# Performance work log

Hardware: AMD Instinct MI355X
Metric: run time of the kernel (lower is better)

Reference implementation:

```python
import jax, jax.numpy as jnp
import numpy as np

SLIDING_WINDOW = 512
LOGIT_SOFTCAP = 50.0
NEG_INF = -1e30


def setup_inputs() -> dict:
    key = jax.random.key(0)
    ks = jax.random.split(key, 3)
    B, S, H, KVH, D, BS = 4, 1024, 32, 8, 128, 64
    nb = S // BS          # blocks per sequence = 16
    nblocks = B * nb      # total cache blocks = 64
    total = B * S         # flattened tokens = 4096
    return {
        "query": jax.random.normal(ks[0], (total, H, D), dtype=jnp.float32),
        "key": jax.random.normal(ks[1], (total, KVH, D), dtype=jnp.float32),
        "value": jax.random.normal(ks[2], (total, KVH, D), dtype=jnp.float32),
        "k_cache": jnp.zeros((nblocks, BS, KVH, D), dtype=jnp.float32),
        "v_cache": jnp.zeros((nblocks, BS, KVH, D), dtype=jnp.float32),
        "block_offsets": jnp.arange(nblocks, dtype=jnp.int32).reshape(B, nb),
    }


def reference(query, key, value, k_cache, v_cache, block_offsets):
    B, nb = block_offsets.shape
    nblocks, BS, KVH, D = k_cache.shape
    S = nb * BS
    H = query.shape[1]
    G = H // KVH  # GQA group size
    scale = D ** -0.5

    flat_blocks = block_offsets.reshape(-1)  # [B*nb]
    # 1) write new keys/values into the paged cache per the block table
    k_cache = k_cache.at[flat_blocks].set(key.reshape(-1, BS, KVH, D))
    v_cache = v_cache.at[flat_blocks].set(value.reshape(-1, BS, KVH, D))
    # 2) gather per-sequence contiguous K/V from cache blocks
    k = k_cache[flat_blocks].reshape(B, S, KVH, D)
    v = v_cache[flat_blocks].reshape(B, S, KVH, D)

    q = query.reshape(B, S, KVH, G, D)
    scores = jnp.einsum("bqhgd,bkhd->bhgqk", q, k) * scale
    # logit softcapping (Gemma-style)
    scores = jnp.tanh(scores / LOGIT_SOFTCAP) * LOGIT_SOFTCAP
    # causal + sliding-window mask
    i = jnp.arange(S)[:, None]
    j = jnp.arange(S)[None, :]
    mask = (j <= i) & ((i - j) < SLIDING_WINDOW)
    scores = jnp.where(mask, scores, NEG_INF)
    p = jax.nn.softmax(scores, axis=-1)
    out = jnp.einsum("bhgqk,bkhd->bqhgd", p, v)
    return out.reshape(B * S, H, D)
```

## Files before the change

kernel.cpp:

```cpp
#include <hip/hip_runtime.h>
#include <hip/hip_bf16.h>

typedef __bf16 bf16_t;
typedef bf16_t bf16x8 __attribute__((ext_vector_type(8)));
typedef bf16_t bf16x4 __attribute__((ext_vector_type(4)));
typedef float f32x4 __attribute__((ext_vector_type(4)));

#define B_   4
#define S_   1024
#define H_   32
#define KVH_ 8
#define D_   128
#define WIN_ 512
#define KVD_ (KVH_ * D_)
#define LOG2E_ 1.4426950408889634f
#define C1_ (2.0f * (0.08838834764831845f / 50.0f) * LOG2E_)
#define K2_ (50.0f * LOG2E_)
#define NK22_ (-2.0f * K2_)
#define EXP2F_(x) __builtin_amdgcn_exp2f(x)

__global__ __launch_bounds__(256) void prep_kv(
    const float* __restrict__ K, const float* __restrict__ V,
    bf16_t* __restrict__ Kb, bf16_t* __restrict__ Vt)
{
  const int j0  = blockIdx.x * 64;
  const int kvh = blockIdx.y;
  const int b   = blockIdx.z;
  const int t   = threadIdx.x;
  const int j   = t >> 2;
  const int d0  = (t & 3) * 32;
  __shared__ bf16_t tl[128][72];

  {
    const float* src = K + (size_t)(b * S_ + j0 + j) * KVD_ + kvh * D_ + d0;
    bf16_t* dst = Kb + ((size_t)(b * KVH_ + kvh) * S_ + j0 + j) * D_ + d0;
    #pragma unroll
    for (int c = 0; c < 4; ++c) {
      float4 f0 = *(const float4*)(src + c * 8);
      float4 f1 = *(const float4*)(src + c * 8 + 4);
      bf16x8 o = { (bf16_t)f0.x, (bf16_t)f0.y, (bf16_t)f0.z, (bf16_t)f0.w,
                   (bf16_t)f1.x, (bf16_t)f1.y, (bf16_t)f1.z, (bf16_t)f1.w };
      *(bf16x8*)(dst + c * 8) = o;
    }
  }
  {
    const float* src = V + (size_t)(b * S_ + j0 + j) * KVD_ + kvh * D_ + d0;
    #pragma unroll
    for (int c = 0; c < 8; ++c) {
      float4 f = *(const float4*)(src + c * 4);
      tl[d0 + c * 4 + 0][j] = (bf16_t)f.x;
      tl[d0 + c * 4 + 1][j] = (bf16_t)f.y;
      tl[d0 + c * 4 + 2][j] = (bf16_t)f.z;
      tl[d0 + c * 4 + 3][j] = (bf16_t)f.w;
    }
  }
  __syncthreads();
  {
    const int d = t >> 1, half = (t & 1) * 32;
    bf16_t* dst = Vt + ((size_t)(b * KVH_ + kvh) * D_ + d) * S_ + j0 + half;
    #pragma unroll
    for (int c = 0; c < 4; ++c)
      *(bf16x8*)(dst + c * 8) = *(bf16x8*)&tl[d][half + c * 8];
  }
}

__global__ __launch_bounds__(512, 4) void attn_fwd(
    const float* __restrict__ Q, const bf16_t* __restrict__ Kb,
    const bf16_t* __restrict__ Vt, float* __restrict__ Out)
{
  const int fid = blockIdx.x + 32 * (blockIdx.y + 8 * (int)blockIdx.z);
  const int swz = (fid & 7) * 128 + (fid >> 3);
  const int i0  = (swz & 31) * 32;
  const int kvh = (swz >> 5) & 7;
  const int b   = swz >> 8;

  const int tid  = threadIdx.x;
  const int w    = tid >> 6;
  const int lane = tid & 63;
  const int m16  = lane & 15;
  const int quad = lane >> 4;
  const int g    = w & 3;
  const int rb   = w >> 2;
  const int h    = kvh * 4 + g;
  const int iw   = i0 + rb * 16;
  const int i    = iw + m16;
  const int sw16 = (m16 >> 1) & 3;

  __shared__ __align__(16) bf16_t KsB[2][32 * 128];
  __shared__ __align__(16) bf16_t VtB[2][128 * 32];
  __shared__ __align__(16) bf16_t PsB[8 * 16 * 32];

  bf16x8 qf[4];
  {
    const float* qp = Q + ((size_t)(b * S_ + iw + m16) * H_ + h) * D_;
    #pragma unroll
    for (int s = 0; s < 4; ++s) {
      const int d0 = 32 * s + 8 * quad;
      float4 f0 = *(const float4*)(qp + d0);
      float4 f1 = *(const float4*)(qp + d0 + 4);
      bf16x8 t = { (bf16_t)f0.x, (bf16_t)f0.y, (bf16_t)f0.z, (bf16_t)f0.w,
                   (bf16_t)f1.x, (bf16_t)f1.y, (bf16_t)f1.z, (bf16_t)f1.w };
      qf[s] = t;
    }
  }

  f32x4 O[8];
  #pragma unroll
  for (int c = 0; c < 8; ++c) O[c] = (f32x4){0.f, 0.f, 0.f, 0.f};
  f32x4 lacc = (f32x4){0.f, 0.f, 0.f, 0.f};

  const bf16_t* khead = Kb + (size_t)(b * KVH_ + kvh) * S_ * D_;
  const bf16_t* vhead = Vt + (size_t)(b * KVH_ + kvh) * D_ * S_;

  const int krow = tid >> 4, kpos = tid & 15;
  const int vd   = tid >> 2, vpos = tid & 3;
  const bf16_t* ksrc = khead + (size_t)krow * D_ + kpos * 8;
  const bf16_t* vsrc = vhead + (size_t)vd * S_ + vpos * 8;
  const int koff = krow * 128 + ((kpos ^ (krow & 15)) << 3);
  const int voff = vd * 32 + ((vpos ^ ((vd >> 1) & 3)) << 3);

  const int t_lo = (i0 >= WIN_) ? ((i0 - (WIN_ - 1)) >> 5) : 0;
  const int t_hi = i0 >> 5;

  {
    int4 kr = *(const int4*)(ksrc + (size_t)t_lo * 32 * D_);
    int4 vr = *(const int4*)(vsrc + t_lo * 32);
    *(int4*)&KsB[0][koff] = kr;
    *(int4*)&VtB[0][voff] = vr;
  }
  __syncthreads();
  int buf = 0;

  for (int tb = t_lo; tb <= t_hi; ++tb) {
    const int j0  = tb * 32;
    const bool pre = (tb < t_hi);
    int4 kr, vr;
    if (pre) {
      kr = *(const int4*)(ksrc + (size_t)(j0 + 32) * D_);
      vr = *(const int4*)(vsrc + (j0 + 32));
    }

    if (!(j0 > iw + 15 || j0 + 31 < iw - (WIN_ - 1))) {
      const bool full = (j0 + 31 <= iw) && (iw + 15 - j0 < WIN_);
      const int pw = w * (16 * 32);

      #pragma unroll
      for (int t4 = 0; t4 < 2; ++t4) {
        f32x4 acc = (f32x4){0.f, 0.f, 0.f, 0.f};
        const int row = 16 * t4 + m16;
        __builtin_amdgcn_s_setprio(1);
        #pragma unroll
        for (int s = 0; s < 4; ++s) {
          bf16x8 a = *(const bf16x8*)&KsB[buf][row * 128 + (((quad + 4 * s) ^ m16) << 3)];
          acc = __builtin_amdgcn_mfma_f32_16x16x32_bf16(a, qf[s], acc, 0, 0, 0);
        }
        __builtin_amdgcn_s_setprio(0);
        bf16x4 pk;
        #pragma unroll
        for (int r = 0; r < 4; ++r) {
          float ez = EXP2F_(acc[r] * C1_);
          float p  = EXP2F_(NK22_ * __builtin_amdgcn_rcpf(ez + 1.f));
          if (!full) {
            const int j = j0 + t4 * 16 + 4 * quad + r;
            p = ((j <= i) && (i - j < WIN_)) ? p : 0.f;
          }
          lacc[r] += p;
          pk[r] = (bf16_t)p;
        }
        const int ch = (2 * t4 + (quad >> 1)) ^ sw16;
        *(bf16x4*)&PsB[pw + m16 * 32 + ch * 8 + (quad & 1) * 4] = pk;
      }
      bf16x8 pa = *(const bf16x8*)&PsB[pw + m16 * 32 + ((quad ^ sw16) << 3)];

      __builtin_amdgcn_s_setprio(1);
      #pragma unroll
      for (int c = 0; c < 8; ++c) {
        const int vrow = 16 * c + m16;
        bf16x8 v = *(const bf16x8*)&VtB[buf][vrow * 32 + ((quad ^ sw16) << 3)];
        O[c] = __builtin_amdgcn_mfma_f32_16x16x32_bf16(pa, v, O[c], 0, 0, 0);
      }
      __builtin_amdgcn_s_setprio(0);
    }

    if (pre) {
      *(int4*)&KsB[buf ^ 1][koff] = kr;
      *(int4*)&VtB[buf ^ 1][voff] = vr;
    }
    __syncthreads();
    buf ^= 1;
  }

  float l_run = lacc[0] + lacc[1] + lacc[2] + lacc[3];
  l_run += __shfl_xor(l_run, 16);
  l_run += __shfl_xor(l_run, 32);

  float* ob = Out + ((size_t)(b * S_ + iw) * H_ + h) * D_;
  #pragma unroll
  for (int r = 0; r < 4; ++r) {
    const int rr = 4 * quad + r;
    const float lr = __shfl(l_run, rr);
    const float linv = __builtin_amdgcn_rcpf(lr);
    float* po = ob + (size_t)rr * (H_ * D_);
    #pragma unroll
    for (int c = 0; c < 8; ++c) po[c * 16 + m16] = O[c][r] * linv;
  }
}

extern "C" void kernel_launch(void* const* d_in, const int* in_sizes, int n_in,
                              void* d_out, int out_size, void* d_ws, size_t ws_size,
                              hipStream_t stream) {
  const float* q = (const float*)d_in[0];
  const float* k = (const float*)d_in[1];
  const float* v = (const float*)d_in[2];
  float* out = (float*)d_out;
  const size_t nkv = (size_t)B_ * KVH_ * S_ * D_;
  bf16_t *kb, *vt;
  if (ws_size >= 2 * nkv * sizeof(bf16_t)) {
    kb = (bf16_t*)d_ws; vt = kb + nkv;
  } else {
    kb = (bf16_t*)d_in[3]; vt = (bf16_t*)d_in[4];
  }
  prep_kv<<<dim3(S_ / 64, KVH_, B_), 256, 0, stream>>>(k, v, kb, vt);
  attn_fwd<<<dim3(S_ / 32, KVH_, B_), 512, 0, stream>>>(q, kb, vt, out);
}
```

Measured before the change: 210.7 us.

## Fuse K/V bf16 conversion and V transpose into attention kernel loads

Removes the separate prep_kv kernel and has the attention kernel read fp32 K and V directly from global memory. Half the threads convert K tiles and half convert and transpose V tiles into swizzled shared memory, and the PV read swizzle is adjusted to match. This saves a kernel launch and the bf16 workspace round trip. In exchange, each attention block now re-reads and re-converts fp32 K/V (twice the bytes of bf16) across the window, and the V stores become narrow 2-element LDS writes.

```diff
diff --git a/kernel.cpp b/kernel.cpp
--- a/kernel.cpp
+++ b/kernel.cpp
@@ -4,6 +4,7 @@
 typedef __bf16 bf16_t;
 typedef bf16_t bf16x8 __attribute__((ext_vector_type(8)));
 typedef bf16_t bf16x4 __attribute__((ext_vector_type(4)));
+typedef bf16_t bf16x2 __attribute__((ext_vector_type(2)));
 typedef float f32x4 __attribute__((ext_vector_type(4)));
 
 #define B_   4
@@ -19,54 +20,9 @@
 #define NK22_ (-2.0f * K2_)
 #define EXP2F_(x) __builtin_amdgcn_exp2f(x)
 
-__global__ __launch_bounds__(256) void prep_kv(
-    const float* __restrict__ K, const float* __restrict__ V,
-    bf16_t* __restrict__ Kb, bf16_t* __restrict__ Vt)
-{
-  const int j0  = blockIdx.x * 64;
-  const int kvh = blockIdx.y;
-  const int b   = blockIdx.z;
-  const int t   = threadIdx.x;
-  const int j   = t >> 2;
-  const int d0  = (t & 3) * 32;
-  __shared__ bf16_t tl[128][72];
-
-  {
-    const float* src = K + (size_t)(b * S_ + j0 + j) * KVD_ + kvh * D_ + d0;
-    bf16_t* dst = Kb + ((size_t)(b * KVH_ + kvh) * S_ + j0 + j) * D_ + d0;
-    #pragma unroll
-    for (int c = 0; c < 4; ++c) {
-      float4 f0 = *(const float4*)(src + c * 8);
-      float4 f1 = *(const float4*)(src + c * 8 + 4);
-      bf16x8 o = { (bf16_t)f0.x, (bf16_t)f0.y, (bf16_t)f0.z, (bf16_t)f0.w,
-                   (bf16_t)f1.x, (bf16_t)f1.y, (bf16_t)f1.z, (bf16_t)f1.w };
-      *(bf16x8*)(dst + c * 8) = o;
-    }
-  }
-  {
-    const float* src = V + (size_t)(b * S_ + j0 + j) * KVD_ + kvh * D_ + d0;
-    #pragma unroll
-    for (int c = 0; c < 8; ++c) {
-      float4 f = *(const float4*)(src + c * 4);
-      tl[d0 + c * 4 + 0][j] = (bf16_t)f.x;
-      tl[d0 + c * 4 + 1][j] = (bf16_t)f.y;
-      tl[d0 + c * 4 + 2][j] = (bf16_t)f.z;
-      tl[d0 + c * 4 + 3][j] = (bf16_t)f.w;
-    }
-  }
-  __syncthreads();
-  {
-    const int d = t >> 1, half = (t & 1) * 32;
-    bf16_t* dst = Vt + ((size_t)(b * KVH_ + kvh) * D_ + d) * S_ + j0 + half;
-    #pragma unroll
-    for (int c = 0; c < 4; ++c)
-      *(bf16x8*)(dst + c * 8) = *(bf16x8*)&tl[d][half + c * 8];
-  }
-}
-
 __global__ __launch_bounds__(512, 4) void attn_fwd(
-    const float* __restrict__ Q, const bf16_t* __restrict__ Kb,
-    const bf16_t* __restrict__ Vt, float* __restrict__ Out)
+    const float* __restrict__ Q, const float* __restrict__ K,
+    const float* __restrict__ V, float* __restrict__ Out)
 {
   const int fid = blockIdx.x + 32 * (blockIdx.y + 8 * (int)blockIdx.z);
   const int swz = (fid & 7) * 128 + (fid >> 3);
@@ -109,36 +65,62 @@
   for (int c = 0; c < 8; ++c) O[c] = (f32x4){0.f, 0.f, 0.f, 0.f};
   f32x4 lacc = (f32x4){0.f, 0.f, 0.f, 0.f};
 
-  const bf16_t* khead = Kb + (size_t)(b * KVH_ + kvh) * S_ * D_;
-  const bf16_t* vhead = Vt + (size_t)(b * KVH_ + kvh) * D_ * S_;
-
-  const int krow = tid >> 4, kpos = tid & 15;
-  const int vd   = tid >> 2, vpos = tid & 3;
-  const bf16_t* ksrc = khead + (size_t)krow * D_ + kpos * 8;
-  const bf16_t* vsrc = vhead + (size_t)vd * S_ + vpos * 8;
-  const int koff = krow * 128 + ((kpos ^ (krow & 15)) << 3);
-  const int voff = vd * 32 + ((vpos ^ ((vd >> 1) & 3)) << 3);
+  const bool isK = (tid < 256);
+  const int krow = tid >> 3;
+  const int kseg = tid & 7;
+  const float* ksrc = K + ((size_t)(b * S_ + krow) * KVH_ + kvh) * D_ + kseg * 16;
+  const int koff0 = krow * 128 + (((2 * kseg)     ^ (krow & 15)) << 3);
+  const int koff1 = krow * 128 + (((2 * kseg + 1) ^ (krow & 15)) << 3);
+  const int vt  = tid & 255;
+  const int tv  = (vt >> 4) * 2;
+  const int mpr = vt & 15;
+  const float* vsrc = V + ((size_t)(b * S_ + tv) * KVH_ + kvh) * D_ + mpr * 8;
+  const int vbase = mpr * 256 + (tv & 7);
+  const int vch   = (tv >> 3) ^ ((mpr >> 1) & 3);
 
   const int t_lo = (i0 >= WIN_) ? ((i0 - (WIN_ - 1)) >> 5) : 0;
   const int t_hi = i0 >> 5;
 
-  {
-    int4 kr = *(const int4*)(ksrc + (size_t)t_lo * 32 * D_);
-    int4 vr = *(const int4*)(vsrc + t_lo * 32);
-    *(int4*)&KsB[0][koff] = kr;
-    *(int4*)&VtB[0][voff] = vr;
-  }
+  float4 r0, r1, r2, r3;
+  auto loadStage = [&](int j0v) {
+    if (isK) {
+      const float* p = ksrc + (size_t)j0v * KVD_;
+      r0 = *(const float4*)(p);      r1 = *(const float4*)(p + 4);
+      r2 = *(const float4*)(p + 8);  r3 = *(const float4*)(p + 12);
+    } else {
+      const float* p = vsrc + (size_t)j0v * KVD_;
+      r0 = *(const float4*)(p);            r1 = *(const float4*)(p + 4);
+      r2 = *(const float4*)(p + KVD_);     r3 = *(const float4*)(p + KVD_ + 4);
+    }
+  };
+  auto writeStage = [&](int bi) {
+    if (isK) {
+      bf16x8 lo = { (bf16_t)r0.x, (bf16_t)r0.y, (bf16_t)r0.z, (bf16_t)r0.w,
+                    (bf16_t)r1.x, (bf16_t)r1.y, (bf16_t)r1.z, (bf16_t)r1.w };
+      bf16x8 hi = { (bf16_t)r2.x, (bf16_t)r2.y, (bf16_t)r2.z, (bf16_t)r2.w,
+                    (bf16_t)r3.x, (bf16_t)r3.y, (bf16_t)r3.z, (bf16_t)r3.w };
+      *(bf16x8*)&KsB[bi][koff0] = lo;
+      *(bf16x8*)&KsB[bi][koff1] = hi;
+    } else {
+      const float av[8] = { r0.x, r0.y, r0.z, r0.w, r1.x, r1.y, r1.z, r1.w };
+      const float bv[8] = { r2.x, r2.y, r2.z, r2.w, r3.x, r3.y, r3.z, r3.w };
+      #pragma unroll
+      for (int e = 0; e < 8; ++e) {
+        bf16x2 pr = { (bf16_t)av[e], (bf16_t)bv[e] };
+        *(bf16x2*)&VtB[bi][vbase + e * 32 + ((vch ^ (e >> 1)) << 3)] = pr;
+      }
+    }
+  };
+
+  loadStage(t_lo * 32);
+  writeStage(0);
   __syncthreads();
   int buf = 0;
 
   for (int tb = t_lo; tb <= t_hi; ++tb) {
     const int j0  = tb * 32;
     const bool pre = (tb < t_hi);
-    int4 kr, vr;
-    if (pre) {
-      kr = *(const int4*)(ksrc + (size_t)(j0 + 32) * D_);
-      vr = *(const int4*)(vsrc + (j0 + 32));
-    }
+    if (pre) loadStage(j0 + 32);
 
     if (!(j0 > iw + 15 || j0 + 31 < iw - (WIN_ - 1))) {
       const bool full = (j0 + 31 <= iw) && (iw + 15 - j0 < WIN_);
@@ -176,16 +158,13 @@
       #pragma unroll
       for (int c = 0; c < 8; ++c) {
         const int vrow = 16 * c + m16;
-        bf16x8 v = *(const bf16x8*)&VtB[buf][vrow * 32 + ((quad ^ sw16) << 3)];
+        bf16x8 v = *(const bf16x8*)&VtB[buf][vrow * 32 + (((quad ^ sw16) ^ (c & 3)) << 3)];
         O[c] = __builtin_amdgcn_mfma_f32_16x16x32_bf16(pa, v, O[c], 0, 0, 0);
       }
       __builtin_amdgcn_s_setprio(0);
     }
 
-    if (pre) {
-      *(int4*)&KsB[buf ^ 1][koff] = kr;
-      *(int4*)&VtB[buf ^ 1][voff] = vr;
-    }
+    if (pre) writeStage(buf ^ 1);
     __syncthreads();
     buf ^= 1;
   }
@@ -213,13 +192,5 @@
   const float* k = (const float*)d_in[1];
   const float* v = (const float*)d_in[2];
   float* out = (float*)d_out;
-  const size_t nkv = (size_t)B_ * KVH_ * S_ * D_;
-  bf16_t *kb, *vt;
-  if (ws_size >= 2 * nkv * sizeof(bf16_t)) {
-    kb = (bf16_t*)d_ws; vt = kb + nkv;
-  } else {
-    kb = (bf16_t*)d_in[3]; vt = (bf16_t*)d_in[4];
-  }
-  prep_kv<<<dim3(S_ / 64, KVH_, B_), 256, 0, stream>>>(k, v, kb, vt);
-  attn_fwd<<<dim3(S_ / 32, KVH_, B_), 512, 0, stream>>>(q, kb, vt, out);
+  attn_fwd<<<dim3(S_ / 32, KVH_, B_), 512, 0, stream>>>(q, k, v, out);
 }
```

After: 210.0 us. Within noise of the previous version (-0.3%).

## Stage K/V tiles with direct global-to-LDS async loads and remap block order

Applied to the files above, without the earlier changes.

Replaces the register-staged K/V tile prefetch with global_load_lds 16-byte direct-to-LDS loads. Because each lane's LDS destination is fixed by wave and lane order, the XOR swizzle moves onto the global source address, and the V-tile read swizzle gains an extra term. The block-to-(batch, head, query-tile) mapping is also reworked to rotate query tiles across workgroups, and the s_setprio hints are dropped. This is meant to cut VGPR pressure and the extra LDS-store instructions. It relies on the loop-end barrier being enough to make the async loads visible, with no explicit vmcnt wait.

```diff
diff --git a/kernel.cpp b/kernel.cpp
--- a/kernel.cpp
+++ b/kernel.cpp
@@ -19,6 +19,12 @@
 #define NK22_ (-2.0f * K2_)
 #define EXP2F_(x) __builtin_amdgcn_exp2f(x)
 
+__device__ __forceinline__ void async16(const bf16_t* g, bf16_t* l) {
+  __builtin_amdgcn_global_load_lds(
+      (const __attribute__((address_space(1))) void*)g,
+      (__attribute__((address_space(3))) void*)l, 16, 0, 0);
+}
+
 __global__ __launch_bounds__(256) void prep_kv(
     const float* __restrict__ K, const float* __restrict__ V,
     bf16_t* __restrict__ Kb, bf16_t* __restrict__ Vt)
@@ -69,10 +75,14 @@
     const bf16_t* __restrict__ Vt, float* __restrict__ Out)
 {
   const int fid = blockIdx.x + 32 * (blockIdx.y + 8 * (int)blockIdx.z);
-  const int swz = (fid & 7) * 128 + (fid >> 3);
-  const int i0  = (swz & 31) * 32;
-  const int kvh = (swz >> 5) & 7;
-  const int b   = swz >> 8;
+  const int x   = fid & 7;
+  const int u   = fid >> 3;
+  const int v   = u >> 5;
+  const int q   = ((u & 31) + (v << 3)) & 31;
+  const int i0  = q * 32;
+  const int hd  = x * 4 + v;
+  const int kvh = hd & 7;
+  const int b   = hd >> 3;
 
   const int tid  = threadIdx.x;
   const int w    = tid >> 6;
@@ -112,33 +122,30 @@
   const bf16_t* khead = Kb + (size_t)(b * KVH_ + kvh) * S_ * D_;
   const bf16_t* vhead = Vt + (size_t)(b * KVH_ + kvh) * D_ * S_;
 
-  const int krow = tid >> 4, kpos = tid & 15;
-  const int vd   = tid >> 2, vpos = tid & 3;
-  const bf16_t* ksrc = khead + (size_t)krow * D_ + kpos * 8;
-  const bf16_t* vsrc = vhead + (size_t)vd * S_ + vpos * 8;
-  const int koff = krow * 128 + ((kpos ^ (krow & 15)) << 3);
-  const int voff = vd * 32 + ((vpos ^ ((vd >> 1) & 3)) << 3);
+  const int krow = tid >> 4;
+  const int kch  = (tid & 15) ^ (krow & 15);
+  const bf16_t* ksrc = khead + (size_t)krow * D_ + kch * 8;
+  const int vd  = tid >> 2;
+  const int vch = (tid & 3) ^ ((vd >> 1) & 3) ^ ((vd >> 4) & 3);
+  const bf16_t* vsrc = vhead + (size_t)vd * S_ + vch * 8;
+  bf16_t* const klds = &KsB[0][0] + w * 512;
+  bf16_t* const vlds = &VtB[0][0] + w * 512;
 
   const int t_lo = (i0 >= WIN_) ? ((i0 - (WIN_ - 1)) >> 5) : 0;
   const int t_hi = i0 >> 5;
 
-  {
-    int4 kr = *(const int4*)(ksrc + (size_t)t_lo * 32 * D_);
-    int4 vr = *(const int4*)(vsrc + t_lo * 32);
-    *(int4*)&KsB[0][koff] = kr;
-    *(int4*)&VtB[0][voff] = vr;
-  }
+  auto stage = [&](int j0v, int bi) {
+    async16(ksrc + (size_t)j0v * D_, klds + bi * (32 * 128));
+    async16(vsrc + j0v,              vlds + bi * (128 * 32));
+  };
+
+  stage(t_lo * 32, 0);
   __syncthreads();
   int buf = 0;
 
   for (int tb = t_lo; tb <= t_hi; ++tb) {
     const int j0  = tb * 32;
-    const bool pre = (tb < t_hi);
-    int4 kr, vr;
-    if (pre) {
-      kr = *(const int4*)(ksrc + (size_t)(j0 + 32) * D_);
-      vr = *(const int4*)(vsrc + (j0 + 32));
-    }
+    if (tb < t_hi) stage(j0 + 32, buf ^ 1);
 
     if (!(j0 > iw + 15 || j0 + 31 < iw - (WIN_ - 1))) {
       const bool full = (j0 + 31 <= iw) && (iw + 15 - j0 < WIN_);
@@ -148,13 +155,11 @@
       for (int t4 = 0; t4 < 2; ++t4) {
         f32x4 acc = (f32x4){0.f, 0.f, 0.f, 0.f};
         const int row = 16 * t4 + m16;
-        __builtin_amdgcn_s_setprio(1);
         #pragma unroll
         for (int s = 0; s < 4; ++s) {
           bf16x8 a = *(const bf16x8*)&KsB[buf][row * 128 + (((quad + 4 * s) ^ m16) << 3)];
           acc = __builtin_amdgcn_mfma_f32_16x16x32_bf16(a, qf[s], acc, 0, 0, 0);
         }
-        __builtin_amdgcn_s_setprio(0);
         bf16x4 pk;
         #pragma unroll
         for (int r = 0; r < 4; ++r) {
@@ -172,20 +177,14 @@
       }
       bf16x8 pa = *(const bf16x8*)&PsB[pw + m16 * 32 + ((quad ^ sw16) << 3)];
 
-      __builtin_amdgcn_s_setprio(1);
       #pragma unroll
       for (int c = 0; c < 8; ++c) {
         const int vrow = 16 * c + m16;
-        bf16x8 v = *(const bf16x8*)&VtB[buf][vrow * 32 + ((quad ^ sw16) << 3)];
-        O[c] = __builtin_amdgcn_mfma_f32_16x16x32_bf16(pa, v, O[c], 0, 0, 0);
+        bf16x8 vv = *(const bf16x8*)&VtB[buf][vrow * 32 + (((quad ^ sw16) ^ (c & 3)) << 3)];
+        O[c] = __builtin_amdgcn_mfma_f32_16x16x32_bf16(pa, vv, O[c], 0, 0, 0);
       }
-      __builtin_amdgcn_s_setprio(0);
-    }
-
-    if (pre) {
-      *(int4*)&KsB[buf ^ 1][koff] = kr;
-      *(int4*)&VtB[buf ^ 1][voff] = vr;
-    }
+    }
+
     __syncthreads();
     buf ^= 1;
   }
```

New measurement: 215.2 us. 2.1% more time.
